# Performance work log

Hardware: AMD Instinct MI355X
Metric: run time of the kernel (lower is better)

## Reference

```python
import jax, jax.numpy as jnp
import numpy as np
import math

B, C, T = 4, 512, 2048
LN_EPS = 1e-5

def setup_inputs() -> dict:
    key = jax.random.key(0)
    ks = jax.random.split(key, 12)
    s = 1.0 / math.sqrt(C)
    inp = {
        'feat': jax.random.normal(ks[0], (B, C, T), dtype=jnp.float32),
        'Wq': jax.random.normal(ks[1], (C, C), dtype=jnp.float32) * s,
        'bq': jax.random.normal(ks[2], (C,), dtype=jnp.float32) * s,
        'Wk': jax.random.normal(ks[3], (C, C), dtype=jnp.float32) * s,
        'bk': jax.random.normal(ks[4], (C,), dtype=jnp.float32) * s,
        'Wv': jax.random.normal(ks[5], (C, C), dtype=jnp.float32) * s,
        'bv': jax.random.normal(ks[6], (C,), dtype=jnp.float32) * s,
        'Ws': jax.random.normal(ks[7], (C, C), dtype=jnp.float32) * s,
        'bs': jax.random.normal(ks[8], (C,), dtype=jnp.float32) * s,
        'Wl': jax.random.normal(ks[9], (C,), dtype=jnp.float32) * s,
        'bl': jax.random.normal(ks[10], (1,), dtype=jnp.float32) * s,
    }
    return inp

def reference(feat, Wq, bq, Wk, bk, Wv, bv, Ws, bs, Wl, bl):
    d = feat.shape[1]
    # 1x1 Conv1d == per-position linear over channels. feat: [B,C,T]
    value = jnp.einsum('oc,bct->bto', Wv, feat) + bv          # [B,T,C]
    query = jnp.einsum('oc,bct->bto', Wq, feat) + bq          # [B,T,C]
    key_  = jnp.einsum('oc,bct->bct', Wk, feat) + bk[:, None] # [B,C,T]
    f = jnp.einsum('btc,bcs->bts', query, key_) / math.sqrt(d)
    f = jax.nn.softmax(f, axis=2)                             # [B,T,T]
    y = jnp.einsum('bts,bsc->btc', f, value)                  # [B,T,C]
    f_score = jax.nn.sigmoid(jnp.einsum('btc,c->bt', y, Wl) + bl[0])
    z = jnp.einsum('bts,bsc->btc', 1.0 - f, value)            # [B,T,C]
    b_score = 1.0 - jax.nn.sigmoid(jnp.einsum('btc,c->bt', z, Wl) + bl[0])
    f_score = (f_score + b_score) / 2.0
    y_ct = jnp.einsum('oc,btc->bot', Ws, y) + bs[:, None]     # smooth conv, [B,C,T]
    out = feat + y_ct
    # LayerNorm over (C, T) jointly, default affine (weight=1, bias=0)
    mu = jnp.mean(out, axis=(1, 2), keepdims=True)
    var = jnp.mean(jnp.square(out - mu), axis=(1, 2), keepdims=True)
    out = (out - mu) * jax.lax.rsqrt(var + LN_EPS)
    return out, f_score
```

## Files before the change

kernel.cpp:

```cpp
#include <hip/hip_runtime.h>
#include <hip/hip_bf16.h>

#define BB 4
#define CC 512
#define TT 2048
static constexpr long CT  = (long)CC * TT;
static constexpr long TC  = (long)TT * CC;
static constexpr long TTT = (long)TT * TT;
static constexpr float SM_SCALE = 0.04419417382415922f;

typedef __bf16 bf16;
typedef __attribute__((ext_vector_type(8))) __bf16 bf16x8;
typedef __attribute__((ext_vector_type(4))) __bf16 bf16x4;
typedef __attribute__((ext_vector_type(4))) float f32x4;

__device__ __forceinline__ void load_lds16(const bf16* g, bf16* l)
{
    __builtin_amdgcn_global_load_lds(
        (const __attribute__((address_space(1))) void*)g,
        (__attribute__((address_space(3))) void*)l, 16, 0, 0);
}

#define FENCE asm volatile("" ::: "memory")

template <int N> __device__ __forceinline__ void vm_wait()
{
    if constexpr (N == 0)       asm volatile("s_waitcnt vmcnt(0)" ::: "memory");
    else if constexpr (N == 4)  asm volatile("s_waitcnt vmcnt(4)" ::: "memory");
    else if constexpr (N == 5)  asm volatile("s_waitcnt vmcnt(5)" ::: "memory");
    else if constexpr (N == 8)  asm volatile("s_waitcnt vmcnt(8)" ::: "memory");
    else if constexpr (N == 10) asm volatile("s_waitcnt vmcnt(10)" ::: "memory");
    else if constexpr (N == 12) asm volatile("s_waitcnt vmcnt(12)" ::: "memory");
    else static_assert(N == 0, "unsupported vmcnt literal");
}

template <int TM, int TN, int WR, int WC, int BK, int DEPTH>
struct CorePipe {
    static constexpr int THREADS = WR * WC * 64;
    static constexpr int MI = TM / (WR * 16);
    static constexpr int NI = TN / (WC * 16);
    static constexpr int CPR = BK / 8;
    static constexpr int RSH = (BK == 64) ? 3 : 2;
    static constexpr int CMASK = CPR - 1;
    static constexpr int CHUNKS = (TM + TN) * CPR;
    static constexpr int ACH = TM * CPR;
    static constexpr int CPT = CHUNKS / THREADS;
    static_assert(CPT * THREADS == CHUNKS, "chunk divisibility");
    static_assert(DEPTH == 2 || DEPTH == 3, "depth 2 or 3");

    __device__ static __forceinline__ void stage(
        const bf16* __restrict__ Ab, const bf16* __restrict__ Bb,
        int K, int m0, int n0, int t, int p, bf16* As, bf16* Bs, int tid)
    {
#pragma unroll
        for (int i = 0; i < CPT; ++i) {
            int c = tid + i * THREADS;
            if (c < ACH) {
                int row = c >> RSH;
                int gc  = (c & CMASK) ^ (row & CMASK);
                load_lds16(Ab + (long)(m0 + row) * K + t * BK + gc * 8,
                           As + p * (TM * BK) + c * 8);
            } else {
                int d = c - ACH;
                int row = d >> RSH;
                int gc  = (d & CMASK) ^ (row & CMASK);
                load_lds16(Bb + (long)(n0 + row) * K + t * BK + gc * 8,
                           Bs + p * (TN * BK) + d * 8);
            }
        }
    }

    __device__ static __forceinline__ void run(
        const bf16* __restrict__ Ab, const bf16* __restrict__ Bb,
        int K, int m0, int n0, bf16* As, bf16* Bs, f32x4 (&acc)[MI][NI])
    {
        const int tid  = threadIdx.x;
        const int lane = tid & 63;
        const int wid  = tid >> 6;
        const int wr = (wid / WC) * (MI * 16);
        const int wc = (wid % WC) * (NI * 16);
        const int lm = lane & 15;
        const int lq = lane >> 4;
        const int nt = K / BK;

#pragma unroll
        for (int d = 0; d < DEPTH; ++d)
            stage(Ab, Bb, K, m0, n0, d, d, As, Bs, tid);
        vm_wait<CPT * (DEPTH - 1)>();
        FENCE; __builtin_amdgcn_s_barrier(); FENCE;

        int p = 0;
        for (int t = 0; t < nt; ++t) {
            const bf16* Ap = As + p * (TM * BK);
            const bf16* Bp = Bs + p * (TN * BK);
            bf16x8 af[BK / 32][MI], bfr[BK / 32][NI];
#pragma unroll
            for (int ks = 0; ks < BK / 32; ++ks) {
#pragma unroll
                for (int i = 0; i < MI; ++i) {
                    int ar = wr + i * 16 + lm;
                    int cc = (ks * 4 + lq) ^ (ar & CMASK);
                    af[ks][i] = *(const bf16x8*)(Ap + ar * BK + cc * 8);
                }
#pragma unroll
                for (int i = 0; i < NI; ++i) {
                    int br = wc + i * 16 + lm;
                    int cc = (ks * 4 + lq) ^ (br & CMASK);
                    bfr[ks][i] = *(const bf16x8*)(Bp + br * BK + cc * 8);
                }
            }
            asm volatile("s_waitcnt lgkmcnt(0)" ::: "memory");
            __builtin_amdgcn_sched_barrier(0);
            FENCE; __builtin_amdgcn_s_barrier(); FENCE;
            if (t + DEPTH < nt)
                stage(Ab, Bb, K, m0, n0, t + DEPTH, p, As, Bs, tid);
            __builtin_amdgcn_s_setprio(1);
#pragma unroll
            for (int ks = 0; ks < BK / 32; ++ks)
#pragma unroll
                for (int mi = 0; mi < MI; ++mi)
#pragma unroll
                    for (int ni = 0; ni < NI; ++ni)
                        acc[mi][ni] = __builtin_amdgcn_mfma_f32_16x16x32_bf16(
                            af[ks][mi], bfr[ks][ni], acc[mi][ni], 0, 0, 0);
            __builtin_amdgcn_s_setprio(0);
            if (t + 1 < nt) {
                const int rem = nt - t;
                if (rem > DEPTH)                    vm_wait<CPT * (DEPTH - 1)>();
                else if (DEPTH == 3 && rem == 3)    vm_wait<CPT>();
                else                                vm_wait<0>();
                FENCE; __builtin_amdgcn_s_barrier(); FENCE;
            }
            p = (p + 1 == DEPTH) ? 0 : p + 1;
        }
    }
};

using CPVS  = CorePipe<128, 128, 4, 2, 64, 3>;
using CPOUT = CorePipe<64, 256, 1, 8, 64, 3>;

struct CoreQVPipe {
    static constexpr int THREADS = 512;
    static constexpr int MI = 2;
    static constexpr int NI = 4;
    static constexpr int BK = 64;
    static constexpr int CPR = 8, RSH = 3, CMASK = 7;
    static constexpr int ACH = 128 * 8;
    static constexpr int CHUNKS = 256 * 8;
    static constexpr int CPT = CHUNKS / THREADS;

    __device__ static __forceinline__ void stage(
        const bf16* __restrict__ Ab, const bf16* __restrict__ Bq,
        const bf16* __restrict__ Bv, int m0, int t, int p,
        bf16* As, bf16* Bs, int tid)
    {
#pragma unroll
        for (int i = 0; i < CPT; ++i) {
            int c = tid + i * THREADS;
            if (c < ACH) {
                int row = c >> RSH;
                int gc  = (c & CMASK) ^ (row & CMASK);
                load_lds16(Ab + (long)(m0 + row) * 512 + t * 64 + gc * 8,
                           As + p * (128 * 64) + c * 8);
            } else {
                int d = c - ACH;
                int row = d >> RSH;
                int gc  = (d & CMASK) ^ (row & CMASK);
                const bf16* src = (row < 64)
                    ? Bq + (long)row * 512
                    : Bv + (long)(row - 64) * 512;
                load_lds16(src + t * 64 + gc * 8, Bs + p * (128 * 64) + d * 8);
            }
        }
    }

    __device__ static __forceinline__ void run(
        const bf16* __restrict__ Ab, const bf16* __restrict__ Bq,
        const bf16* __restrict__ Bv,
        int m0, bf16* As, bf16* Bs, f32x4 (&acc)[MI][NI])
    {
        const int tid  = threadIdx.x;
        const int lane = tid & 63;
        const int wid  = tid >> 6;
        const int wr = (wid / 2) * 32;
        const int wc = (wid % 2) * 64;
        const int lm = lane & 15;
        const int lq = lane >> 4;
        const int nt = 8;

        stage(Ab, Bq, Bv, m0, 0, 0, As, Bs, tid);
        stage(Ab, Bq, Bv, m0, 1, 1, As, Bs, tid);
        vm_wait<4>();
        FENCE; __builtin_amdgcn_s_barrier(); FENCE;

        for (int t = 0; t < nt; ++t) {
            const int p = t & 1;
            const bf16* Ap = As + p * (128 * 64);
            const bf16* Bp = Bs + p * (128 * 64);
            bf16x8 af[2][MI], bfr[2][NI];
#pragma unroll
            for (int ks = 0; ks < 2; ++ks) {
#pragma unroll
                for (int i = 0; i < MI; ++i) {
                    int ar = wr + i * 16 + lm;
                    int cc = (ks * 4 + lq) ^ (ar & CMASK);
                    af[ks][i] = *(const bf16x8*)(Ap + ar * BK + cc * 8);
                }
#pragma unroll
                for (int i = 0; i < NI; ++i) {
                    int br = wc + i * 16 + lm;
                    int cc = (ks * 4 + lq) ^ (br & CMASK);
                    bfr[ks][i] = *(const bf16x8*)(Bp + br * BK + cc * 8);
                }
            }
            asm volatile("s_waitcnt lgkmcnt(0)" ::: "memory");
            __builtin_amdgcn_sched_barrier(0);
            FENCE; __builtin_amdgcn_s_barrier(); FENCE;
            if (t + 2 < nt)
                stage(Ab, Bq, Bv, m0, t + 2, p, As, Bs, tid);
            __builtin_amdgcn_s_setprio(1);
#pragma unroll
            for (int ks = 0; ks < 2; ++ks)
#pragma unroll
                for (int mi = 0; mi < MI; ++mi)
#pragma unroll
                    for (int ni = 0; ni < NI; ++ni)
                        acc[mi][ni] = __builtin_amdgcn_mfma_f32_16x16x32_bf16(
                            af[ks][mi], bfr[ks][ni], acc[mi][ni], 0, 0, 0);
            __builtin_amdgcn_s_setprio(0);
            if (t + 1 < nt) {
                if (t + 2 < nt) vm_wait<4>();
                else            vm_wait<0>();
                FENCE; __builtin_amdgcn_s_barrier(); FENCE;
            }
        }
    }
};

__global__ __launch_bounds__(512)
void gemm_qv_kernel(const bf16* __restrict__ featT, const bf16* __restrict__ Wq_bf,
                    const bf16* __restrict__ Wv_bf, bf16* __restrict__ Qb,
                    bf16* __restrict__ Vn, const float* __restrict__ bq,
                    const float* __restrict__ bv, const float* __restrict__ wkc,
                    const float* __restrict__ bk, float* __restrict__ qb,
                    const float* __restrict__ Wl, float* __restrict__ vl)
{
    __shared__ __align__(16) bf16 As[2 * 128 * 64];
    __shared__ __align__(16) bf16 Bs[2 * 128 * 64];
    const int rb = blockIdx.z;
    const int m0 = blockIdx.y * 128;
    const int ng = blockIdx.x;
    const long wofs = (long)(ng * 64) * 512;
    f32x4 acc[2][4] = {};
    CoreQVPipe::run(featT + (long)rb * TC, Wq_bf + wofs, Wv_bf + wofs, m0, As, Bs, acc);

    const int lane = threadIdx.x & 63, wid = threadIdx.x >> 6;
    const int wr = (wid / 2) * 32;
    const bool isV = wid & 1;
    const int lm = lane & 15, lq = lane >> 4;

    if (isV) {
        bf16* outV = Vn + (long)rb * TC;
        float* vlb = vl + (long)rb * TT;
        float vs_[2][4] = {};
#pragma unroll
        for (int mi = 0; mi < 2; ++mi)
#pragma unroll
            for (int ni = 0; ni < 4; ++ni) {
                int n = ng * 64 + ni * 16 + lm;
                float bn = bv[n], wn = Wl[n];
#pragma unroll
                for (int r = 0; r < 4; ++r) {
                    int m = m0 + wr + mi * 16 + lq * 4 + r;
                    float v = acc[mi][ni][r] + bn;
                    outV[(long)m * 512 + n] = (bf16)v;
                    vs_[mi][r] += v * wn;
                }
            }
#pragma unroll
        for (int mi = 0; mi < 2; ++mi)
#pragma unroll
            for (int r = 0; r < 4; ++r) {
                float s = vs_[mi][r];
                s += __shfl_xor(s, 1, 64); s += __shfl_xor(s, 2, 64);
                s += __shfl_xor(s, 4, 64); s += __shfl_xor(s, 8, 64);
                if (lm == 0)
                    atomicAdd(vlb + m0 + wr + mi * 16 + lq * 4 + r, s);
            }
    } else {
        bf16* out = Qb + (long)rb * TC;
        float* qbb = qb + (long)rb * TT;
        float rs[2][4] = {};
#pragma unroll
        for (int mi = 0; mi < 2; ++mi)
#pragma unroll
            for (int ni = 0; ni < 4; ++ni) {
                int n = ng * 64 + ni * 16 + lm;
                float bn = bq[n], wn = wkc[n], kn = bk[n];
#pragma unroll
                for (int r = 0; r < 4; ++r) {
                    int m = m0 + wr + mi * 16 + lq * 4 + r;
                    float v = acc[mi][ni][r] + bn;
                    rs[mi][r] += v * kn;
                    out[(long)m * 512 + n] = (bf16)(v * wn);
                }
            }
#pragma unroll
        for (int mi = 0; mi < 2; ++mi)
#pragma unroll
            for (int r = 0; r < 4; ++r) {
                float s = rs[mi][r];
                s += __shfl_xor(s, 1, 64); s += __shfl_xor(s, 2, 64);
                s += __shfl_xor(s, 4, 64); s += __shfl_xor(s, 8, 64);
                if (lm == 0)
                    atomicAdd(qbb + m0 + wr + mi * 16 + lq * 4 + r, s);
            }
    }
}

__global__ __launch_bounds__(512, 2)
void gemm_s256_kernel(const bf16* __restrict__ Qb, const bf16* __restrict__ featT,
                      bf16* __restrict__ S, const float* __restrict__ qb,
                      float* __restrict__ rsum, const float* __restrict__ vl,
                      float* __restrict__ u)
{
    __shared__ __align__(16) bf16 lds[2][2][256 * 64];
    const int id   = blockIdx.x;
    const int xcd  = id & 7, sIdx = id >> 3;
    const int bz   = xcd >> 1;
    const int n0   = (sIdx & 7) * 256;
    const int m0   = (((xcd & 1) << 2) + (sIdx >> 3)) * 256;
    const bf16* __restrict__ Ab = Qb + (long)bz * TC;
    const bf16* __restrict__ Bb = featT + (long)bz * TC;

    const int tid  = threadIdx.x;
    const int lane = tid & 63;
    const int wid  = tid >> 6;
    const int lm = lane & 15, lq = lane >> 4;
    const int wrb = (wid >> 2) * 64;
    const int wcb = (wid & 3) * 32;

    f32x4 acc[8][4] = {};

#define STAGE_HT(t, op, h)                                                    \
    do {                                                                      \
        const bf16* gp_ = (op) ? Bb : Ab;                                     \
        const int  br_  = ((op) ? n0 : m0) + (h) * 128;                       \
        bf16* lp_ = &lds[(t) & 1][op][(h) * 128 * 64];                        \
        _Pragma("unroll")                                                     \
        for (int i_ = 0; i_ < 2; ++i_) {                                      \
            int c_ = tid + i_ * 512;                                          \
            int r_ = c_ >> 3;                                                 \
            int g_ = (c_ & 7) ^ (r_ & 7);                                     \
            load_lds16(gp_ + (long)(br_ + r_) * 512 + (t) * 64 + g_ * 8,      \
                       lp_ + c_ * 8);                                         \
        }                                                                     \
    } while (0)

#define PHASE(t, qm, qn, doSt, st, sop, sh, doVm)                             \
    do {                                                                      \
        bf16x8 af[2][4], bfr[2][2];                                           \
        const bf16* Al_ = lds[(t) & 1][0];                                    \
        const bf16* Bl_ = lds[(t) & 1][1];                                    \
        _Pragma("unroll")                                                     \
        for (int ks = 0; ks < 2; ++ks) {                                      \
            _Pragma("unroll")                                                 \
            for (int j = 0; j < 4; ++j) {                                     \
                int ar = (qm) * 128 + wrb + j * 16 + lm;                      \
                int cc = (ks * 4 + lq) ^ (ar & 7);                            \
                af[ks][j] = *(const bf16x8*)(Al_ + ar * 64 + cc * 8);         \
            }                                                                 \
            _Pragma("unroll")                                                 \
            for (int j = 0; j < 2; ++j) {                                     \
                int br = (qn) * 128 + wcb + j * 16 + lm;                      \
                int cc = (ks * 4 + lq) ^ (br & 7);                            \
                bfr[ks][j] = *(const bf16x8*)(Bl_ + br * 64 + cc * 8);        \
            }                                                                 \
        }                                                                     \
        if (doSt) STAGE_HT(st, sop, sh);                                      \
        if (doVm) {                                                           \
            if ((t) < 6) asm volatile("s_waitcnt vmcnt(4)" ::: "memory");     \
            else         asm volatile("s_waitcnt vmcnt(0)" ::: "memory");     \
        }                                                                     \
        FENCE; __builtin_amdgcn_s_barrier(); FENCE;                           \
        __builtin_amdgcn_s_setprio(1);                                        \
        _Pragma("unroll")                                                     \
        for (int ks = 0; ks < 2; ++ks)                                        \
            _Pragma("unroll")                                                 \
            for (int j = 0; j < 4; ++j)                                       \
                _Pragma("unroll")                                             \
                for (int j2 = 0; j2 < 2; ++j2)                                \
                    acc[(qm) * 4 + j][(qn) * 2 + j2] =                        \
                        __builtin_amdgcn_mfma_f32_16x16x32_bf16(              \
                            af[ks][j], bfr[ks][j2],                           \
                            acc[(qm) * 4 + j][(qn) * 2 + j2], 0, 0, 0);       \
        __builtin_amdgcn_s_setprio(0);                                        \
        FENCE; __builtin_amdgcn_s_barrier(); FENCE;                           \
    } while (0)

    STAGE_HT(0, 0, 0); STAGE_HT(0, 1, 0); STAGE_HT(0, 0, 1); STAGE_HT(0, 1, 1);
    STAGE_HT(1, 0, 0); STAGE_HT(1, 1, 0);
    asm volatile("s_waitcnt vmcnt(4)" ::: "memory");
    FENCE; __builtin_amdgcn_s_barrier(); FENCE;

    for (int t = 0; t < 8; ++t) {
        PHASE(t, 0, 0, t + 1 < 8, t + 1, 0, 1, false);
        PHASE(t, 0, 1, t + 1 < 8, t + 1, 1, 1, false);
        PHASE(t, 1, 0, t + 2 < 8, t + 2, 0, 0, false);
        PHASE(t, 1, 1, t + 2 < 8, t + 2, 1, 0, true);
    }
#undef PHASE
#undef STAGE_HT

    bf16* outp = S + (long)bz * TTT;
    const float* qbb = qb + (long)bz * TT;
    const float* vlb = vl + (long)bz * TT;
    float* rsb = rsum + (long)bz * TT;
    float* ub  = u + (long)bz * TT;
#pragma unroll
    for (int mi = 0; mi < 8; ++mi) {
        const int mrow = m0 + (mi >> 2) * 128 + wrb + (mi & 3) * 16 + lq * 4;
        const f32x4 qv = *(const f32x4*)(qbb + mrow);
        float rp[4] = {0.f, 0.f, 0.f, 0.f};
        float up[4] = {0.f, 0.f, 0.f, 0.f};
#pragma unroll
        for (int ni = 0; ni < 4; ++ni) {
            const int ncol = n0 + (ni >> 1) * 128 + wcb + (ni & 1) * 16 + lm;
            const float vlv = vlb[ncol];
#pragma unroll
            for (int r = 0; r < 4; ++r) {
                float p = __expf((acc[mi][ni][r] + qv[r]) * SM_SCALE);
                outp[(long)(mrow + r) * 2048 + ncol] = (bf16)p;
                rp[r] += p;
                up[r] += p * vlv;
            }
        }
#pragma unroll
        for (int r = 0; r < 4; ++r) {
            float s2 = rp[r], s3 = up[r];
            s2 += __shfl_xor(s2, 1, 64); s2 += __shfl_xor(s2, 2, 64);
            s2 += __shfl_xor(s2, 4, 64); s2 += __shfl_xor(s2, 8, 64);
            s3 += __shfl_xor(s3, 1, 64); s3 += __shfl_xor(s3, 2, 64);
            s3 += __shfl_xor(s3, 4, 64); s3 += __shfl_xor(s3, 8, 64);
            if (lm == 0) {
                atomicAdd(rsb + mrow + r, s2);
                atomicAdd(ub + mrow + r, s3);
            }
        }
    }
}

__global__ __launch_bounds__(512)
void gemm_vs_kernel(const bf16* __restrict__ Vn, const bf16* __restrict__ Ws_bf,
                    bf16* __restrict__ Vpt)
{
    __shared__ __align__(16) bf16 As[3 * 128 * 64];
    __shared__ __align__(16) bf16 Bs[3 * 128 * 64];
    const int id = blockIdx.x;
    const int xcd = id & 7, s = id >> 3;
    const int bz = xcd >> 1;
    const int m0 = (((xcd & 1) << 1) + (s >> 4)) * 128;
    const int n0 = (s & 15) * 128;
    f32x4 acc[2][4] = {};
    CPVS::run(Ws_bf, Vn + (long)bz * TC, 512, m0, n0, As, Bs, acc);

    const int lane = threadIdx.x & 63, wid = threadIdx.x >> 6;
    const int wr = (wid / 2) * 32, wc = (wid % 2) * 64;
    const int lm = lane & 15, lq = lane >> 4;
    bf16* out = Vpt + (long)bz * CT;
#pragma unroll
    for (int mi = 0; mi < 2; ++mi)
#pragma unroll
        for (int ni = 0; ni < 4; ++ni) {
            int n = n0 + wc + ni * 16 + lm;
#pragma unroll
            for (int r = 0; r < 4; ++r) {
                int m = m0 + wr + mi * 16 + lq * 4 + r;
                out[(long)m * 2048 + n] = (bf16)acc[mi][ni][r];
            }
        }
}

__global__ __launch_bounds__(512)
void gemm_out_kernel(const bf16* __restrict__ S, const bf16* __restrict__ Vpt,
                     float* __restrict__ out, const float* __restrict__ bs,
                     const float* __restrict__ feat,
                     const float* __restrict__ rsum, double* __restrict__ stats)
{
    __shared__ __align__(16) bf16 As[3 * 64 * 64];
    __shared__ __align__(16) bf16 Bs[3 * 256 * 64];
    __shared__ float red[16];
    const int id = blockIdx.x;
    const int xcd = id & 7, sIdx = id >> 3;
    const int bz = xcd >> 1;
    const int n0 = (sIdx & 1) * 256;
    const int m0 = (((xcd & 1) << 4) + (sIdx >> 1)) * 64;
    f32x4 acc[4][2] = {};
    CPOUT::run(S + (long)bz * TTT, Vpt + (long)bz * CT, 2048, m0, n0, As, Bs, acc);

    const int tid = threadIdx.x;
    const int lane = tid & 63, wid = tid >> 6;
    const int lm = lane & 15, lq = lane >> 4;
    const float* rsb = rsum + (long)bz * TT;
    float inv[4][4];
#pragma unroll
    for (int mi = 0; mi < 4; ++mi) {
        int mrow = m0 + mi * 16 + lq * 4;
        f32x4 rv = *(const f32x4*)(rsb + mrow);
#pragma unroll
        for (int r = 0; r < 4; ++r) inv[mi][r] = 1.f / rv[r];
    }
    float s1 = 0.f, s2 = 0.f;
#pragma unroll
    for (int mi = 0; mi < 4; ++mi)
#pragma unroll
        for (int ni = 0; ni < 2; ++ni) {
            int mrow = m0 + mi * 16 + lq * 4;
            int n = n0 + wid * 32 + ni * 16 + lm;
            long off = (long)bz * CT + (long)n * TT + mrow;
            f32x4 fv = *(const f32x4*)(feat + off);
            float bn = bs[n];
            f32x4 res;
#pragma unroll
            for (int r = 0; r < 4; ++r) {
                float v = acc[mi][ni][r] * inv[mi][r] + bn + fv[r];
                res[r] = v;
                s1 += v;
                s2 += v * v;
            }
            *(f32x4*)(out + off) = res;
        }
#pragma unroll
    for (int off = 32; off; off >>= 1) {
        s1 += __shfl_xor(s1, off, 64);
        s2 += __shfl_xor(s2, off, 64);
    }
    if (lane == 0) { red[wid] = s1; red[8 + wid] = s2; }
    __syncthreads();
    if (tid == 0) {
        double t1 = 0.0, t2 = 0.0;
#pragma unroll
        for (int w = 0; w < 8; ++w) { t1 += red[w]; t2 += red[8 + w]; }
        atomicAdd(stats + bz * 2, t1);
        atomicAdd(stats + bz * 2 + 1, t2);
    }
}

__global__ __launch_bounds__(256)
void prep_kernel(const float* __restrict__ feat, bf16* __restrict__ featT,
                 const float* __restrict__ Wq, const float* __restrict__ Wv,
                 const float* __restrict__ Ws, bf16* __restrict__ Wbf,
                 const float* __restrict__ Wk, const float* __restrict__ Wl,
                 const float* __restrict__ bv, float* __restrict__ wkc,
                 float* __restrict__ wvl, float* __restrict__ wlbv,
                 float* __restrict__ frp, float* __restrict__ qb,
                 float* __restrict__ u, float* __restrict__ rsum,
                 double* __restrict__ stats, float* __restrict__ vl)
{
    const int blk = blockIdx.x;
    const int tid = threadIdx.x;
    if (blk < 4096) {
        __shared__ float tile[32][33];
        __shared__ float sfr[4][32];
        const int b  = blk >> 10;
        const int c0 = ((blk & 1023) >> 6) * 32;
        const int tt = blk & 63;
        const int t0 = tt * 32;
        const int tx = tid & 31;
        const int ty = tid >> 5;
#pragma unroll
        for (int j = 0; j < 4; ++j) {
            int c = c0 + ty + j * 8;
            tile[ty + j * 8][tx] = feat[(long)b * CT + (long)c * TT + t0 + tx];
        }
        __syncthreads();
        float ps = 0.f;
#pragma unroll
        for (int j = 0; j < 4; ++j) {
            int tl = ty + j * 8;
            int t = t0 + tl;
            int c = c0 + tx;
            float v = tile[tx][tl];
            ps += v;
            featT[(long)b * TC + (long)t * CC + c] = (bf16)v;
        }
        const int wid = tid >> 6;
        ps += __shfl_xor(ps, 32, 64);
        if ((tid & 63) < 32) sfr[wid][tx] = ps;
        __syncthreads();
        if (tid < 32) {
            float s = sfr[0][tid] + sfr[1][tid] + sfr[2][tid] + sfr[3][tid];
            frp[(((long)b * 64 + tt) << 9) + c0 + tid] = s;
        }
    } else if (blk < 4480) {
        long gid = (long)(blk - 4096) * 256 + tid;
        long idx = gid * 8;
        int w = (int)(idx >> 18);
        long off = idx & 262143;
        const float* src = (w == 0) ? Wq : (w == 1) ? Wv : Ws;
        f32x4 a = *(const f32x4*)(src + off);
        f32x4 b = *(const f32x4*)(src + off + 4);
        bf16x8 o;
#pragma unroll
        for (int j = 0; j < 4; ++j) { o[j] = (bf16)a[j]; o[4 + j] = (bf16)b[j]; }
        *(bf16x8*)(Wbf + idx) = o;
    } else {
        int mid = (blk - 4480) * 256 + tid;
        if (mid < 512) {
            float s = 0.f;
            for (int o = 0; o < 512; ++o) s += Wk[o * 512 + mid];
            wkc[mid] = s;
        } else if (mid < 1024) {
            int k = mid - 512;
            float s = 0.f;
            for (int c = 0; c < 512; ++c) s += Wl[c] * Wv[c * 512 + k];
            wvl[k] = s;
        } else if (mid < 1088) {
            int lane = mid - 1024;
            float s = 0.f;
#pragma unroll
            for (int j = 0; j < 8; ++j) s += Wl[lane + 64 * j] * bv[lane + 64 * j];
#pragma unroll
            for (int off = 32; off; off >>= 1) s += __shfl_xor(s, off, 64);
            if (lane == 0) wlbv[0] = s;
        } else if (mid >= 1152 && mid < 1160) {
            stats[mid - 1152] = 0.0;
        } else if (mid >= 4096 && mid < 12288) {
            qb[mid - 4096] = 0.f;
        } else if (mid >= 12288 && mid < 20480) {
            u[mid - 12288] = 0.f;
        } else if (mid >= 20480 && mid < 28672) {
            rsum[mid - 20480] = 0.f;
        } else if (mid >= 28672 && mid < 36864) {
            vl[mid - 28672] = 0.f;
        }
    }
}

__global__ __launch_bounds__(256)
void ln_score_kernel(float* __restrict__ out, const double* __restrict__ stats,
                     const float* __restrict__ u, const float* __restrict__ frp,
                     const float* __restrict__ wvl, const float* __restrict__ wlbv,
                     const float* __restrict__ blp, const float* __restrict__ rsum)
{
    if (blockIdx.x < 4096) {
        long i = ((long)blockIdx.x * 256 + threadIdx.x) * 4;
        int b = (int)(i >> 20);
        const double n = 1048576.0;
        double mu  = stats[b * 2] / n;
        double var = stats[b * 2 + 1] / n - mu * mu;
        float rs = (float)(1.0 / sqrt(var + 1e-5));
        float muf = (float)mu;
        f32x4 v = *(f32x4*)(out + i);
#pragma unroll
        for (int j = 0; j < 4; ++j) v[j] = (v[j] - muf) * rs;
        *(f32x4*)(out + i) = v;
    } else {
        const int b = blockIdx.x - 4096;
        __shared__ float ssv[4];
        const int tid = threadIdx.x, lane = tid & 63, wid = tid >> 6;
        const float* fb = frp + ((long)b * 64 << 9);
        float s0 = 0.f, s1 = 0.f;
#pragma unroll 8
        for (int k = 0; k < 64; ++k) {
            s0 += fb[(k << 9) + tid];
            s1 += fb[(k << 9) + tid + 256];
        }
        float p = s0 * wvl[tid] + s1 * wvl[tid + 256];
#pragma unroll
        for (int off = 32; off; off >>= 1) p += __shfl_xor(p, off, 64);
        if (lane == 0) ssv[wid] = p;
        __syncthreads();
        const float sv = ssv[0] + ssv[1] + ssv[2] + ssv[3] + 2048.f * wlbv[0];
        const float bl0 = blp[0];
#pragma unroll
        for (int j = 0; j < 8; ++j) {
            int t = tid + j * 256;
            float uu = u[(long)b * TT + t] / rsum[(long)b * TT + t];
            float uf = uu + bl0;
            float vf = sv - uu + bl0;
            float fs  = 1.f / (1.f + __expf(-uf));
            float bsc = 1.f - 1.f / (1.f + __expf(-vf));
            out[(long)BB * CT + (long)b * TT + t] = 0.5f * (fs + bsc);
        }
    }
}

extern "C" void kernel_launch(void* const* d_in, const int* in_sizes, int n_in,
                              void* d_out, int out_size, void* d_ws, size_t ws_size,
                              hipStream_t stream)
{
    const float* feat = (const float*)d_in[0];
    const float* Wq   = (const float*)d_in[1];
    const float* bq   = (const float*)d_in[2];
    const float* Wk   = (const float*)d_in[3];
    const float* bk   = (const float*)d_in[4];
    const float* Wv   = (const float*)d_in[5];
    const float* bv   = (const float*)d_in[6];
    const float* Ws   = (const float*)d_in[7];
    const float* bs   = (const float*)d_in[8];
    const float* Wl   = (const float*)d_in[9];
    const float* bl   = (const float*)d_in[10];
    float* out = (float*)d_out;

    if (ws_size < 69316736) return;
    char* ws = (char*)d_ws;
    bf16* featT  = (bf16*)(ws);
    bf16* Wbf    = (bf16*)(ws + 8388608);
    bf16* Qb     = (bf16*)(ws + 9961472);
    bf16* Vn     = (bf16*)(ws + 18350080);
    bf16* Vpt    = (bf16*)(ws + 26738688);
    float* vl    = (float*)(ws + 26738688);
    bf16* S      = (bf16*)(ws + 35127296);
    float* wkc   = (float*)(ws + 68689920);
    float* wvl   = (float*)(ws + 68691968);
    float* wlbv  = (float*)(ws + 68694016);
    float* qb    = (float*)(ws + 68694080);
    double* stats= (double*)(ws + 68726848);
    float* u     = (float*)(ws + 68726912);
    float* rsum  = (float*)(ws + 68759680);
    float* frp   = (float*)(ws + 68792448);

    bf16* Wq_bf = Wbf;
    bf16* Wv_bf = Wbf + 262144;
    bf16* Ws_bf = Wbf + 524288;

    prep_kernel<<<4624, 256, 0, stream>>>(feat, featT, Wq, Wv, Ws, Wbf, Wk, Wl, bv,
                                          wkc, wvl, wlbv, frp, qb, u, rsum, stats, vl);
    gemm_qv_kernel<<<dim3(8, 16, 4), 512, 0, stream>>>(
        featT, Wq_bf, Wv_bf, Qb, Vn, bq, bv, wkc, bk, qb, Wl, vl);
    gemm_s256_kernel<<<256, 512, 0, stream>>>(Qb, featT, S, qb, rsum, vl, u);
    gemm_vs_kernel<<<256, 512, 0, stream>>>(Vn, Ws_bf, Vpt);
    gemm_out_kernel<<<256, 512, 0, stream>>>(S, Vpt, out, bs, feat, rsum, stats);
    ln_score_kernel<<<4100, 256, 0, stream>>>(out, stats, u, frp, wvl, wlbv, bl, rsum);
}
```

Measured before the change: 215.0 us.

## Merge score GEMM and value-smoothing GEMM into one launch; use double buffering

```diff
diff --git a/kernel.cpp b/kernel.cpp
--- a/kernel.cpp
+++ b/kernel.cpp
@@ -30,7 +30,6 @@
     else if constexpr (N == 5)  asm volatile("s_waitcnt vmcnt(5)" ::: "memory");
     else if constexpr (N == 8)  asm volatile("s_waitcnt vmcnt(8)" ::: "memory");
     else if constexpr (N == 10) asm volatile("s_waitcnt vmcnt(10)" ::: "memory");
-    else if constexpr (N == 12) asm volatile("s_waitcnt vmcnt(12)" ::: "memory");
     else static_assert(N == 0, "unsupported vmcnt literal");
 }
 
@@ -136,8 +135,8 @@
     }
 };
 
-using CPVS  = CorePipe<128, 128, 4, 2, 64, 3>;
-using CPOUT = CorePipe<64, 256, 1, 8, 64, 3>;
+using CPVS  = CorePipe<128, 128, 4, 2, 64, 2>;
+using CPOUT = CorePipe<64, 256, 1, 8, 64, 2>;
 
 struct CoreQVPipe {
     static constexpr int THREADS = 512;
@@ -319,12 +318,45 @@
 }
 
 __global__ __launch_bounds__(512, 2)
-void gemm_s256_kernel(const bf16* __restrict__ Qb, const bf16* __restrict__ featT,
-                      bf16* __restrict__ S, const float* __restrict__ qb,
-                      float* __restrict__ rsum, const float* __restrict__ vl,
-                      float* __restrict__ u)
+void gemm_mid_kernel(const bf16* __restrict__ Qb, const bf16* __restrict__ featT,
+                     bf16* __restrict__ S, const float* __restrict__ qb,
+                     float* __restrict__ rsum, const float* __restrict__ vl,
+                     float* __restrict__ u, const bf16* __restrict__ Vn,
+                     const bf16* __restrict__ Ws_bf, bf16* __restrict__ Vpt)
 {
     __shared__ __align__(16) bf16 lds[2][2][256 * 64];
+    const int tid  = threadIdx.x;
+    const int lane = tid & 63;
+    const int wid  = tid >> 6;
+    const int lm = lane & 15, lq = lane >> 4;
+
+    if (blockIdx.x >= 256) {
+        const int id2 = blockIdx.x - 256;
+        const int xcd = id2 & 7, s = id2 >> 3;
+        const int bz = xcd >> 1;
+        const int m0 = (((xcd & 1) << 1) + (s >> 4)) * 128;
+        const int n0 = (s & 15) * 128;
+        bf16* As = &lds[0][0][0];
+        bf16* Bs = &lds[0][1][0];
+        f32x4 acc[2][4] = {};
+        CPVS::run(Ws_bf, Vn + (long)bz * TC, 512, m0, n0, As, Bs, acc);
+
+        const int wr = (wid / 2) * 32, wc = (wid % 2) * 64;
+        bf16* outp = Vpt + (long)bz * CT;
+#pragma unroll
+        for (int mi = 0; mi < 2; ++mi)
+#pragma unroll
+            for (int ni = 0; ni < 4; ++ni) {
+                int n = n0 + wc + ni * 16 + lm;
+#pragma unroll
+                for (int r = 0; r < 4; ++r) {
+                    int m = m0 + wr + mi * 16 + lq * 4 + r;
+                    outp[(long)m * 2048 + n] = (bf16)acc[mi][ni][r];
+                }
+            }
+        return;
+    }
+
     const int id   = blockIdx.x;
     const int xcd  = id & 7, sIdx = id >> 3;
     const int bz   = xcd >> 1;
@@ -333,10 +365,6 @@
     const bf16* __restrict__ Ab = Qb + (long)bz * TC;
     const bf16* __restrict__ Bb = featT + (long)bz * TC;
 
-    const int tid  = threadIdx.x;
-    const int lane = tid & 63;
-    const int wid  = tid >> 6;
-    const int lm = lane & 15, lq = lane >> 4;
     const int wrb = (wid >> 2) * 64;
     const int wcb = (wid & 3) * 32;
 
@@ -451,44 +479,13 @@
 }
 
 __global__ __launch_bounds__(512)
-void gemm_vs_kernel(const bf16* __restrict__ Vn, const bf16* __restrict__ Ws_bf,
-                    bf16* __restrict__ Vpt)
-{
-    __shared__ __align__(16) bf16 As[3 * 128 * 64];
-    __shared__ __align__(16) bf16 Bs[3 * 128 * 64];
-    const int id = blockIdx.x;
-    const int xcd = id & 7, s = id >> 3;
-    const int bz = xcd >> 1;
-    const int m0 = (((xcd & 1) << 1) + (s >> 4)) * 128;
-    const int n0 = (s & 15) * 128;
-    f32x4 acc[2][4] = {};
-    CPVS::run(Ws_bf, Vn + (long)bz * TC, 512, m0, n0, As, Bs, acc);
-
-    const int lane = threadIdx.x & 63, wid = threadIdx.x >> 6;
-    const int wr = (wid / 2) * 32, wc = (wid % 2) * 64;
-    const int lm = lane & 15, lq = lane >> 4;
-    bf16* out = Vpt + (long)bz * CT;
-#pragma unroll
-    for (int mi = 0; mi < 2; ++mi)
-#pragma unroll
-        for (int ni = 0; ni < 4; ++ni) {
-            int n = n0 + wc + ni * 16 + lm;
-#pragma unroll
-            for (int r = 0; r < 4; ++r) {
-                int m = m0 + wr + mi * 16 + lq * 4 + r;
-                out[(long)m * 2048 + n] = (bf16)acc[mi][ni][r];
-            }
-        }
-}
-
-__global__ __launch_bounds__(512)
 void gemm_out_kernel(const bf16* __restrict__ S, const bf16* __restrict__ Vpt,
                      float* __restrict__ out, const float* __restrict__ bs,
                      const float* __restrict__ feat,
                      const float* __restrict__ rsum, double* __restrict__ stats)
 {
-    __shared__ __align__(16) bf16 As[3 * 64 * 64];
-    __shared__ __align__(16) bf16 Bs[3 * 256 * 64];
+    __shared__ __align__(16) bf16 As[2 * 64 * 64];
+    __shared__ __align__(16) bf16 Bs[2 * 256 * 64];
     __shared__ float red[16];
     const int id = blockIdx.x;
     const int xcd = id & 7, sIdx = id >> 3;
@@ -703,14 +700,13 @@
     const float* bl   = (const float*)d_in[10];
     float* out = (float*)d_out;
 
-    if (ws_size < 69316736) return;
+    if (ws_size < 69349504) return;
     char* ws = (char*)d_ws;
     bf16* featT  = (bf16*)(ws);
     bf16* Wbf    = (bf16*)(ws + 8388608);
     bf16* Qb     = (bf16*)(ws + 9961472);
     bf16* Vn     = (bf16*)(ws + 18350080);
     bf16* Vpt    = (bf16*)(ws + 26738688);
-    float* vl    = (float*)(ws + 26738688);
     bf16* S      = (bf16*)(ws + 35127296);
     float* wkc   = (float*)(ws + 68689920);
     float* wvl   = (float*)(ws + 68691968);
@@ -720,6 +716,7 @@
     float* u     = (float*)(ws + 68726912);
     float* rsum  = (float*)(ws + 68759680);
     float* frp   = (float*)(ws + 68792448);
+    float* vl    = (float*)(ws + 69316736);
 
     bf16* Wq_bf = Wbf;
     bf16* Wv_bf = Wbf + 262144;
@@ -729,8 +726,8 @@
                                           wkc, wvl, wlbv, frp, qb, u, rsum, stats, vl);
     gemm_qv_kernel<<<dim3(8, 16, 4), 512, 0, stream>>>(
         featT, Wq_bf, Wv_bf, Qb, Vn, bq, bv, wkc, bk, qb, Wl, vl);
-    gemm_s256_kernel<<<256, 512, 0, stream>>>(Qb, featT, S, qb, rsum, vl, u);
-    gemm_vs_kernel<<<256, 512, 0, stream>>>(Vn, Ws_bf, Vpt);
+    gemm_mid_kernel<<<512, 512, 0, stream>>>(Qb, featT, S, qb, rsum, vl, u,
+                                             Vn, Ws_bf, Vpt);
     gemm_out_kernel<<<256, 512, 0, stream>>>(S, Vpt, out, bs, feat, rsum, stats);
     ln_score_kernel<<<4100, 256, 0, stream>>>(out, stats, u, frp, wvl, wlbv, bl, rsum);
 }
```

After: 212.1 us. No clear change (-1.4%).
